# Kernel tuning notes

Hardware: AMD Instinct MI355X
Metric: run time of the kernel (lower is better)

Reference implementation:

```python
import jax, jax.numpy as jnp
import numpy as np

B, T, D, V, U = 16, 1000, 512, 5000, 64


def _safe_logaddexp(a, b):
    # logaddexp with nan-safe gradients when both args are -inf
    both = jnp.isneginf(a) & jnp.isneginf(b)
    a_ = jnp.where(both, 0.0, a)
    b_ = jnp.where(both, 0.0, b)
    return jnp.where(both, -jnp.inf, jnp.logaddexp(a_, b_))


def _log_sub_exp(a, b):
    # faithful port of log_substraction_exp: log(exp(a) - exp(b)), stable
    mask1 = (~jnp.isinf(a)) & (~jnp.isinf(b))
    a_ = jnp.where(mask1, a, -1.0)
    b_ = jnp.where(mask1, b, -2.0)
    ans_tmp = b_ + jnp.log(jnp.exp(a_ - b_) - 1.0)
    a_ = jnp.where(jnp.isinf(ans_tmp), -2000.0, a_)
    b_ = jnp.where(jnp.isinf(ans_tmp), -2001.0, b_)
    ans1 = b_ + jnp.log(jnp.exp(a_ - b_) - 1.0)
    ans = jnp.where(mask1, ans1, -jnp.inf)
    mask2 = (~jnp.isinf(a)) & jnp.isinf(b)
    return jnp.where(mask2, a, ans)


def _ctc_trellis(logp, ys):
    # Standard CTC lattice over extended labels (blank interleaved), S = 2U+1.
    # alpha[t,b,s]: logprob of paths over frames 0..t ending in state s (incl. emission at t)
    # beta[t,b,s]:  logprob of emitting frames t+1..T-1 and finishing, given state s at t
    # This reproduces the k2 lattice forward/backward scores at the label states.
    Bb, Tt, _ = logp.shape
    Uu = ys.shape[1]
    S = 2 * Uu + 1
    l_ext = jnp.zeros((Bb, S), ys.dtype).at[:, 1::2].set(ys)  # blank=0 at even s
    lp = jnp.take_along_axis(logp, jnp.broadcast_to(l_ext[:, None, :], (Bb, Tt, S)), axis=2)
    skip_ok = jnp.zeros((Bb, S), bool).at[:, 3::2].set(ys[:, 1:] != ys[:, :-1])
    lpT = jnp.transpose(lp, (1, 0, 2))  # [T,B,S]
    ninf1 = jnp.full((Bb, 1), -jnp.inf)
    ninf2 = jnp.full((Bb, 2), -jnp.inf)

    a0 = jnp.full((Bb, S), -jnp.inf).at[:, :2].set(lpT[0, :, :2])

    def astep(ap, lp_t):
        s1 = jnp.concatenate([ninf1, ap[:, :-1]], 1)
        s2 = jnp.concatenate([ninf2, ap[:, :-2]], 1)
        a = lp_t + _safe_logaddexp(_safe_logaddexp(ap, s1), jnp.where(skip_ok, s2, -jnp.inf))
        return a, a

    _, arest = jax.lax.scan(astep, a0, lpT[1:])
    alpha = jnp.concatenate([a0[None], arest], 0)  # [T,B,S]

    bl = jnp.full((Bb, S), -jnp.inf).at[:, S - 2:].set(0.0)  # final states: last label / last blank
    skipL2 = jnp.concatenate([skip_ok[:, 2:], jnp.zeros((Bb, 2), bool)], 1)

    def bstep(bn, lp_next):
        m = lp_next + bn
        m1 = jnp.concatenate([m[:, 1:], ninf1], 1)
        m2 = jnp.concatenate([m[:, 2:], ninf2], 1)
        bcur = _safe_logaddexp(_safe_logaddexp(m, m1), jnp.where(skipL2, m2, -jnp.inf))
        return bcur, bcur

    _, brest = jax.lax.scan(bstep, bl, lpT[1:], reverse=True)
    beta = jnp.concatenate([brest, bl[None]], 0)  # [T,B,S]
    return alpha, beta, lp


def setup_inputs() -> dict:
    key = jax.random.key(0)
    k1, k2, k3 = jax.random.split(key, 3)
    hs_pad = jax.random.normal(k1, (B, T, D), jnp.float32)
    hlens = jnp.full((B,), T, jnp.int32)
    ys_pad = jax.random.randint(k2, (B, U), 1, V)  # labels in [1, V); 0 is blank
    ali = jnp.zeros((B, U), jnp.int32)  # unused when risk_factor == 0
    W = jax.random.normal(k3, (D, V), jnp.float32) * 0.02
    b = jnp.zeros((V,), jnp.float32)
    return {"hs_pad": hs_pad, "hlens": hlens, "ys_pad": ys_pad, "ali": ali, "W": W, "b": b}


def reference(hs_pad, hlens, ys_pad, ali, W, b):
    # ctc_lo + log_softmax (dropout_rate=0). hlens are all equal -> sort/unsort is identity.
    logp = jax.nn.log_softmax(hs_pad @ W + b, axis=-1)  # [B,T,V]
    alpha_f, beta_f, lp = _ctc_trellis(logp, ys_pad)
    alpha = jnp.transpose(alpha_f[:, :, 1::2], (1, 2, 0))  # [B,U,T]
    beta = jnp.transpose(beta_f[:, :, 1::2], (1, 2, 0))    # [B,U,T]
    p = jnp.transpose(lp[:, :, 1::2], (0, 2, 1))           # [B,U,T] logprob of label u at frame t
    # beta', excluding re-emission of label u at t+1 -> paths whose label-u segment ends at t
    bp = _log_sub_exp(beta[:, :, :-1], beta[:, :, 1:] + p[:, :, 1:])
    bp = jnp.concatenate([bp, beta[:, :, -1:]], -1)
    loss_state = alpha + bp
    loss_state = jnp.where(jnp.isnan(loss_state), -jnp.inf, loss_state)
    loss_u = jax.nn.logsumexp(loss_state, axis=2)  # aggregate == 'time'
    mask = jnp.isinf(loss_u)
    denom = (~mask).astype(loss_u.dtype).sum(1)
    loss_fsas = jnp.where(mask, 0.0, loss_u).sum(1) / denom
    Uu = ys_pad.shape[1]
    loss_fsas = jnp.where(hlens < Uu, 0.0, loss_fsas)
    return (-loss_fsas).mean()
```

## Files before the change

### kernel.cpp

```cpp
#include <hip/hip_runtime.h>

#define NB 16
#define NT 1000
#define ND 512
#define NV 5000
#define NVP 5120
#define NU 64
#define NLL 66
#define NWG 72
#define NM (NB * NT)
#define NCH 40

typedef short short8v __attribute__((ext_vector_type(8)));
typedef float float4v __attribute__((ext_vector_type(4)));

#define NEGINF (-__builtin_inff())
#define SENTL  (-1.0e30f)
#define LOG2E 1.4426950408889634f
#define LN2F  0.6931471805599453f
#define SENT2 (-2000.4586751f * LOG2E)

__device__ __forceinline__ float fexp2(float x) { return __builtin_amdgcn_exp2f(x); }
__device__ __forceinline__ float flog2(float x) { return __builtin_amdgcn_logf(x); }

__device__ __forceinline__ float dpp_shr1(float x) {
  int xi = __builtin_bit_cast(int, x);
  int r = __builtin_amdgcn_update_dpp(xi, xi, 0x138, 0xf, 0xf, false);
  return __builtin_bit_cast(float, r);
}
__device__ __forceinline__ float dpp_shl1(float x) {
  int xi = __builtin_bit_cast(int, x);
  int r = __builtin_amdgcn_update_dpp(xi, xi, 0x130, 0xf, 0xf, false);
  return __builtin_bit_cast(float, r);
}

__device__ __forceinline__ short f2bf(float x) {
  unsigned int u = __builtin_bit_cast(unsigned int, x);
  unsigned int r = (u + 0x7fffu + ((u >> 16) & 1u)) >> 16;
  return (short)(unsigned short)r;
}
__device__ __forceinline__ float bf2f(short h) {
  unsigned int u = ((unsigned int)(unsigned short)h) << 16;
  return __builtin_bit_cast(float, u);
}

__device__ __forceinline__ void g2lds16(const short* g, short* l) {
  __builtin_amdgcn_global_load_lds(
      (const __attribute__((address_space(1))) void*)g,
      (__attribute__((address_space(3))) void*)l, 16, 0, 0);
}

__device__ __forceinline__ float lae2s(float a, float b) {
  float m = fmaxf(a, b);
  return m + flog2(fexp2(a - m) + fexp2(b - m));
}
__device__ __forceinline__ float lae3s(float a, float b, float c) {
  float m = fmaxf(fmaxf(a, b), c);
  return m + flog2(fexp2(a - m) + fexp2(b - m) + fexp2(c - m));
}
__device__ __forceinline__ float lsub2(float a, float b) {
  if (b < -1.0e29f) return (a < -1.0e29f) ? SENTL : a;
  float tmp = b + flog2(fexp2(a - b) - 1.0f);
  if (__builtin_isinf(tmp)) tmp = SENT2;
  return tmp;
}

__global__ __launch_bounds__(256) void k_cvt(const float* __restrict__ hs,
                                             const float* __restrict__ W,
                                             short* __restrict__ hsb,
                                             short* __restrict__ WT,
                                             short* __restrict__ WTlo,
                                             float* __restrict__ outv) {
  __shared__ short tileH[64 * 72];
  __shared__ short tileL[64 * 72];
  if (blockIdx.x < 4000) {
    if (blockIdx.x == 0 && threadIdx.x == 0) outv[0] = 0.0f;
    size_t i = (size_t)blockIdx.x * 256 + threadIdx.x;
    const float4* p = (const float4*)hs + i * 2;
    float4 v0 = p[0], v1 = p[1];
    short8v r;
    r[0] = f2bf(v0.x); r[1] = f2bf(v0.y); r[2] = f2bf(v0.z); r[3] = f2bf(v0.w);
    r[4] = f2bf(v1.x); r[5] = f2bf(v1.y); r[6] = f2bf(v1.z); r[7] = f2bf(v1.w);
    int row = (int)(i >> 6);
    int g = (int)(i & 63);
    int gs = (g & ~7) | ((g & 7) ^ (row & 7));
    *(short8v*)(hsb + (size_t)row * ND + gs * 8) = r;
    return;
  }
  int bx = blockIdx.x - 4000;
  int n0 = (bx % 80) * 64, k0 = (bx / 80) * 64;
  int tid = threadIdx.x;
  int kr = tid >> 2, part = tid & 3;
  const float* src = W + (size_t)(k0 + kr) * NV + n0 + part * 16;
#pragma unroll
  for (int jj = 0; jj < 4; ++jj) {
    int c = n0 + part * 16 + jj * 4;
    float4 v;
    if (c + 3 < NV) {
      v = *(const float4*)(src + jj * 4);
    } else {
      v.x = (c + 0 < NV) ? src[jj * 4 + 0] : 0.f;
      v.y = (c + 1 < NV) ? src[jj * 4 + 1] : 0.f;
      v.z = (c + 2 < NV) ? src[jj * 4 + 2] : 0.f;
      v.w = (c + 3 < NV) ? src[jj * 4 + 3] : 0.f;
    }
    int base = kr * 72 + part * 16 + jj * 4;
    float vv[4] = {v.x, v.y, v.z, v.w};
#pragma unroll
    for (int q = 0; q < 4; ++q) {
      short h = f2bf(vv[q]);
      tileH[base + q] = h;
      tileL[base + q] = f2bf(vv[q] - bf2f(h));
    }
  }
  __syncthreads();
  int n = tid & 63, kq = tid >> 6;
  int nn = n0 + n;
  if (nn < NVP) {
#pragma unroll
    for (int half = 0; half < 2; ++half) {
      short8v vh, vl;
#pragma unroll
      for (int jj = 0; jj < 8; ++jj) {
        vh[jj] = tileH[(kq * 16 + half * 8 + jj) * 72 + n];
        vl[jj] = tileL[(kq * 16 + half * 8 + jj) * 72 + n];
      }
      int g = (k0 >> 3) + kq * 2 + half;
      int gs = (g & ~7) | ((g & 7) ^ (nn & 7));
      *(short8v*)(WT + (size_t)nn * ND + gs * 8) = vh;
      *(short8v*)(WTlo + (size_t)nn * ND + gs * 8) = vl;
    }
  }
}

__global__ __launch_bounds__(64) void k_gather2(const short* __restrict__ WT,
                                                const short* __restrict__ WTlo,
                                                const int* __restrict__ ys,
                                                short* __restrict__ Wg_hi,
                                                short* __restrict__ Wg_lo) {
  int u = blockIdx.x, b = blockIdx.y, t = threadIdx.x;
  short8v hi = {0,0,0,0,0,0,0,0}, lo = {0,0,0,0,0,0,0,0};
  if (u < NU + 1) {
    int lab = (u == 0) ? 0 : ys[b * NU + u - 1];
    int ps = (t & ~7) | ((t & 7) ^ (lab & 7));
    hi = *(const short8v*)(WT + (size_t)lab * ND + ps * 8);
    lo = *(const short8v*)(WTlo + (size_t)lab * ND + ps * 8);
  }
  int q = (t & ~7) | ((t & 7) ^ (u & 7));
  size_t base = ((size_t)(b * NWG + u)) * ND + q * 8;
  *(short8v*)(Wg_hi + base) = hi;
  *(short8v*)(Wg_lo + base) = lo;
}

__global__ __launch_bounds__(256) void k_labg(const short* __restrict__ hsb,
                                              const short* __restrict__ Wg_hi,
                                              const short* __restrict__ Wg_lo,
                                              const int* __restrict__ ys,
                                              const float* __restrict__ bias,
                                              float* __restrict__ ll) {
  __shared__ short As[128 * 64];
  __shared__ short Bh[128 * 64];
  __shared__ short Bl[128 * 64];

  int mt = blockIdx.x, b = blockIdx.y;
  int t0 = mt * 128;
  int tid = threadIdx.x;
  int lane = tid & 63, wave = tid >> 6;
  int wm = wave >> 1, wn = wave & 1;
  int lrow = lane & 15, lkhi = lane >> 4;

  const short* gaBase = hsb + (size_t)(b * NT + t0 + wave * 32 + (lane >> 3)) * ND + (lane & 7) * 8;

  float4v acc[4][4];
#pragma unroll
  for (int m = 0; m < 4; ++m)
#pragma unroll
    for (int n = 0; n < 4; ++n)
#pragma unroll
      for (int j = 0; j < 4; ++j) acc[m][n][j] = 0.f;

  for (int s = 0; s < 8; ++s) {
    int k0 = s * 64;
#pragma unroll
    for (int i = 0; i < 4; ++i) {
      g2lds16(gaBase + (size_t)(i * 8) * ND + k0, &As[(wave * 32 + i * 8) * 64]);
      int brow = wave * 32 + (lane >> 3) + i * 8;
      int brc = (brow < NWG - 1) ? brow : (NWG - 1);
      g2lds16(Wg_hi + (size_t)(b * NWG + brc) * ND + (lane & 7) * 8 + k0,
              &Bh[(wave * 32 + i * 8) * 64]);
      g2lds16(Wg_lo + (size_t)(b * NWG + brc) * ND + (lane & 7) * 8 + k0,
              &Bl[(wave * 32 + i * 8) * 64]);
    }
    __syncthreads();
#pragma unroll
    for (int kk = 0; kk < 2; ++kk) {
      short8v av[4], bhv[4], blv2[4];
#pragma unroll
      for (int m = 0; m < 4; ++m) {
        int r = wm * 64 + m * 16 + lrow;
        int col = (kk * 32 + lkhi * 8) ^ ((r & 7) << 3);
        av[m] = *(const short8v*)&As[r * 64 + col];
      }
#pragma unroll
      for (int n = 0; n < 4; ++n) {
        int r = wn * 64 + n * 16 + lrow;
        int col = (kk * 32 + lkhi * 8) ^ ((r & 7) << 3);
        bhv[n] = *(const short8v*)&Bh[r * 64 + col];
        blv2[n] = *(const short8v*)&Bl[r * 64 + col];
      }
#pragma unroll
      for (int m = 0; m < 4; ++m)
#pragma unroll
        for (int n = 0; n < 4; ++n) {
          acc[m][n] = __builtin_amdgcn_mfma_f32_16x16x32_bf16(av[m], bhv[n], acc[m][n], 0, 0, 0);
          acc[m][n] = __builtin_amdgcn_mfma_f32_16x16x32_bf16(av[m], blv2[n], acc[m][n], 0, 0, 0);
        }
    }
    __syncthreads();
  }

  float bu[4]; bool uval[4];
#pragma unroll
  for (int n = 0; n < 4; ++n) {
    int u = wn * 64 + n * 16 + lrow;
    uval[n] = u < NU + 1;
    int lab = (u == 0) ? 0 : (uval[n] ? ys[b * NU + u - 1] : 0);
    bu[n] = uval[n] ? bias[lab] : 0.f;
  }
#pragma unroll
  for (int m = 0; m < 4; ++m)
#pragma unroll
    for (int j = 0; j < 4; ++j) {
      int trow = t0 + wm * 64 + m * 16 + lkhi * 4 + j;
      if (trow < NT) {
#pragma unroll
        for (int n = 0; n < 4; ++n) {
          int u = wn * 64 + n * 16 + lrow;
          if (uval[n])
            ll[((size_t)(b * NLL + u)) * NT + trow] = acc[m][n][j] + bu[n];
        }
      }
    }
}

__global__ __launch_bounds__(256) void k_big(const short* __restrict__ hsb,
                                             const short* __restrict__ WT,
                                             const float* __restrict__ bias,
                                             const float* __restrict__ ll,
                                             const int* __restrict__ ys,
                                             float* __restrict__ L,
                                             float* __restrict__ aod) {
  __shared__ short As[128 * 64];
  __shared__ short Ws[128 * 64];
  __shared__ float mred[128][2];
  __shared__ float sred[128][2];

  int bid = blockIdx.x;
  int tid = threadIdx.x;

  if (bid < NB) {
    float* pbS = (float*)As;
    int b = bid;
    const float* llb = ll + (size_t)b * NLL * NT;
    for (int i = tid; i < NT; i += 256) pbS[i] = llb[i] * LOG2E;
    __syncthreads();
    if (tid >= 64) return;
    int l = tid;
    const float* lrow = llb + (size_t)(1 + l) * NT;

    int lab = ys[b * NU + l];
    int labp = ys[b * NU + ((l >= 1) ? (l - 1) : 0)];
    bool skip = (l >= 1) && (lab != labp);
    float* aodb = aod + (size_t)b * NT * NU;

    float ae = (l == 0) ? pbS[0] : SENTL;
    float ao = (l == 0) ? lrow[0] * LOG2E : SENTL;
    aodb[l] = ao;

    float cl[16], pbr[16];
#pragma unroll
    for (int j = 0; j < 16; ++j) {
      int tt = 1 + j; if (tt > NT - 1) tt = NT - 1;
      cl[j] = lrow[tt];
      pbr[j] = pbS[tt];
    }
    for (int g = 0; g < 63; ++g) {
      float nl[16], pb2[16];
      if (g < 62) {
#pragma unroll
        for (int j = 0; j < 16; ++j) {
          int tt = 17 + g * 16 + j; if (tt > NT - 1) tt = NT - 1;
          nl[j] = lrow[tt];
          pb2[j] = pbS[tt];
        }
      } else {
#pragma unroll
        for (int j = 0; j < 16; ++j) { nl[j] = 0.f; pb2[j] = 0.f; }
      }
#pragma unroll
      for (int j = 0; j < 16; ++j) {
        int t = 1 + g * 16 + j;
        if (t < NT) {
          float pb = pbr[j];
          float pl = cl[j] * LOG2E;
          float po = dpp_shr1(ao); if (l == 0) po = SENTL;
          float aen = pb + lae2s(ae, po);
          float aon = pl + lae3s(ao, ae, skip ? po : SENTL);
          ae = aen; ao = aon;
          aodb[t * NU + l] = ao;
        }
      }
#pragma unroll
      for (int j = 0; j < 16; ++j) { cl[j] = nl[j]; pbr[j] = pb2[j]; }
    }
    return;
  }

  int lin = bid - NB;
  int o = (lin & 7) * 625 + (lin >> 3);
  int mt, chunk;
  if (o < 4800) {
    int sb = o / 320, w = o % 320;
    mt = sb * 8 + (w & 7);
    chunk = w >> 3;
  } else {
    int w = o - 4800;
    mt = 120 + (w % 5);
    chunk = w / 5;
  }
  int t0 = mt * 128;
  int n0 = chunk * 128;
  int lane = tid & 63, wave = tid >> 6;
  int wm = wave >> 1, wn = wave & 1;
  int lrow = lane & 15, lkhi = lane >> 4;

  const short* gaBase = hsb + (size_t)(t0 + wave * 32 + (lane >> 3)) * ND + (lane & 7) * 8;
  const short* gwBase = WT + (size_t)(n0 + wave * 32 + (lane >> 3)) * ND + (lane & 7) * 8;

  float4v acc[4][4];
#pragma unroll
  for (int m = 0; m < 4; ++m)
#pragma unroll
    for (int n = 0; n < 4; ++n)
#pragma unroll
      for (int j = 0; j < 4; ++j) acc[m][n][j] = 0.f;

  for (int s = 0; s < 8; ++s) {
    int k0 = s * 64;
#pragma unroll
    for (int i = 0; i < 4; ++i) {
      g2lds16(gaBase + (size_t)(i * 8) * ND + k0, &As[(wave * 32 + i * 8) * 64]);
      g2lds16(gwBase + (size_t)(i * 8) * ND + k0, &Ws[(wave * 32 + i * 8) * 64]);
    }
    __syncthreads();
#pragma unroll
    for (int kk = 0; kk < 2; ++kk) {
      short8v av[4], wv[4];
#pragma unroll
      for (int m = 0; m < 4; ++m) {
        int r = wm * 64 + m * 16 + lrow;
        int col = (kk * 32 + lkhi * 8) ^ ((r & 7) << 3);
        av[m] = *(const short8v*)&As[r * 64 + col];
      }
#pragma unroll
      for (int n = 0; n < 4; ++n) {
        int r = wn * 64 + n * 16 + lrow;
        int col = (kk * 32 + lkhi * 8) ^ ((r & 7) << 3);
        wv[n] = *(const short8v*)&Ws[r * 64 + col];
      }
#pragma unroll
      for (int m = 0; m < 4; ++m)
#pragma unroll
        for (int n = 0; n < 4; ++n)
          acc[m][n] = __builtin_amdgcn_mfma_f32_16x16x32_bf16(av[m], wv[n], acc[m][n], 0, 0, 0);
    }
    __syncthreads();
  }

  float bcol[4]; bool cval[4];
#pragma unroll
  for (int n = 0; n < 4; ++n) {
    int c = n0 + wn * 64 + n * 16 + lrow;
    cval[n] = c < NV;
    bcol[n] = cval[n] ? bias[c] : 0.f;
  }
#pragma unroll
  for (int m = 0; m < 4; ++m)
#pragma unroll
    for (int j = 0; j < 4; ++j) {
      float mx = NEGINF;
#pragma unroll
      for (int n = 0; n < 4; ++n) {
        float v = cval[n] ? acc[m][n][j] + bcol[n] : NEGINF;
        mx = fmaxf(mx, v);
      }
#pragma unroll
      for (int d = 1; d < 16; d <<= 1) mx = fmaxf(mx, __shfl_xor(mx, d));
      float mxc = fmaxf(mx, -3.0e38f);
      float p = 0.f;
#pragma unroll
      for (int n = 0; n < 4; ++n) {
        float v = cval[n] ? acc[m][n][j] + bcol[n] : NEGINF;
        p += __expf(v - mxc);
      }
#pragma unroll
      for (int d = 1; d < 16; d <<= 1) p += __shfl_xor(p, d);
      if (lrow == 0) {
        int rloc = wm * 64 + m * 16 + lkhi * 4 + j;
        mred[rloc][wn] = mx;
        sred[rloc][wn] = p;
      }
    }
  __syncthreads();
  if (tid < 128) {
    int row = t0 + tid;
    float m0 = mred[tid][0], m1 = mred[tid][1];
    float m = fmaxf(m0, m1);
    float ss = 0.f;
    if (m != NEGINF)
      ss = ((m0 == NEGINF) ? 0.f : sred[tid][0] * __expf(m0 - m))
         + ((m1 == NEGINF) ? 0.f : sred[tid][1] * __expf(m1 - m));
    float Lv = (m == NEGINF || ss <= 0.f) ? NEGINF : m + __logf(ss);
    L[(size_t)chunk * NM + row] = Lv;
  }
}

__global__ __launch_bounds__(256) void k_dred(const float* __restrict__ L,
                                              float* __restrict__ dnm) {
  int row = blockIdx.x * 256 + threadIdx.x;
  if (row >= NM) return;
  float m40 = NEGINF;
#pragma unroll
  for (int c = 0; c < NCH; ++c) m40 = fmaxf(m40, L[(size_t)c * NM + row]);
  float s = 0.f;
#pragma unroll
  for (int c = 0; c < NCH; ++c) {
    float Lc = L[(size_t)c * NM + row];
    if (Lc > -1.0e29f) s += __expf(Lc - m40);
  }
  dnm[row] = m40 + __logf(s);
}

__global__ __launch_bounds__(256) void k_bwd(const float* __restrict__ ll,
                                             const float* __restrict__ dnm,
                                             const int* __restrict__ ys,
                                             float* __restrict__ bp) {
  __shared__ float dnS[NT];
  __shared__ float pbS[NT];
  int b = blockIdx.x;
  int tid = threadIdx.x;
  const float* llb = ll + (size_t)b * NLL * NT;
  const float* dnb = dnm + b * NT;
  for (int t = tid; t < NT; t += 256) {
    float d = dnb[t];
    float blk = llb[t];
    dnS[t] = d;
    pbS[t] = (blk - d) * LOG2E;
  }
  __syncthreads();
  if (tid >= 64) return;
  int l = tid;
  const float* lrow = llb + (size_t)(1 + l) * NT;

  int lab = ys[b * NU + l];
  int labn = ys[b * NU + ((l < NU - 1) ? (l + 1) : l)];
  bool skipn = (l < NU - 1) && (labn != lab);
  float* bpb = bp + (size_t)b * NT * NU;

  float bo = (l == NU - 1) ? 0.0f : SENTL;
  float be = SENTL;
  float b128 = 0.0f;
  bpb[(NT - 1) * NU + l] = bo;

  float cl[16], pbr[16], dnr[16];
#pragma unroll
  for (int j = 0; j < 16; ++j) {
    int tt = NT - 2 - j; if (tt < 0) tt = 0;
    cl[j] = lrow[tt + 1];
    pbr[j] = pbS[tt + 1];
    dnr[j] = dnS[tt + 1];
  }
  for (int g = 0; g < 63; ++g) {
    float nl2[16], pb2[16], dn2[16];
    if (g < 62) {
#pragma unroll
      for (int j = 0; j < 16; ++j) {
        int tt = NT - 2 - 16 * (g + 1) - j; if (tt < 0) tt = 0;
        nl2[j] = lrow[tt + 1];
        pb2[j] = pbS[tt + 1];
        dn2[j] = dnS[tt + 1];
      }
    } else {
#pragma unroll
      for (int j = 0; j < 16; ++j) { nl2[j] = 0.f; pb2[j] = 0.f; dn2[j] = 0.f; }
    }
#pragma unroll
    for (int j = 0; j < 16; ++j) {
      int t = NT - 2 - 16 * g - j;
      if (t >= 0) {
        float pbv = pbr[j];
        float plv = (cl[j] - dnr[j]) * LOG2E;
        float me = pbv + be;
        float mo = plv + bo;
        float m128 = pbv + b128;
        float ne = dpp_shl1(me); if (l == NU - 1) ne = m128;
        float no = dpp_shl1(mo); if (l == NU - 1) no = SENTL;
        float ben = lae2s(me, mo);
        float bon = lae3s(mo, ne, skipn ? no : SENTL);
        bpb[t * NU + l] = lsub2(bon, mo);
        be = ben; bo = bon; b128 = m128;
      }
    }
#pragma unroll
    for (int j = 0; j < 16; ++j) { cl[j] = nl2[j]; pbr[j] = pb2[j]; dnr[j] = dn2[j]; }
  }
}

__global__ __launch_bounds__(512) void k_loss(const float* __restrict__ aod,
                                              const float* __restrict__ bp,
                                              const float* __restrict__ dnm,
                                              const int* __restrict__ hlens,
                                              float* __restrict__ out) {
  __shared__ float denL[NT];
  __shared__ float Dpre[NT];
  __shared__ float choff[64];
  __shared__ float ms[8][64], ss[8][64];
  int b = blockIdx.x, tid = threadIdx.x;
  for (int t = tid; t < NT; t += 512) denL[t] = dnm[b * NT + t];
  __syncthreads();
  if (tid < 64) {
    float s = 0.f;
#pragma unroll
    for (int i = 0; i < 16; ++i) { int t = tid * 16 + i; if (t < NT) s += denL[t]; }
    float v = s;
#pragma unroll
    for (int d = 1; d < 64; d <<= 1) { float u = __shfl_up(v, d); if (tid >= d) v += u; }
    choff[tid] = v - s;
  }
  __syncthreads();
  for (int t = tid; t < NT; t += 512) {
    float s = choff[t >> 4];
    int base = t & ~15;
    for (int i = base; i <= t; ++i) s += denL[i];
    Dpre[t] = s;
  }
  __syncthreads();
  int w = tid >> 6, l = tid & 63;
  const float* ab = aod + (size_t)b * NT * NU;
  const float* pbp = bp + (size_t)b * NT * NU;
  float m = NEGINF, s = 0.f;
  int t0 = w * 125, t1 = t0 + 125;
  for (int t = t0; t < t1; ++t) {
    float av = ab[t * NU + l];
    float pv = pbp[t * NU + l];
    float x = av - Dpre[t] * LOG2E + pv;
    if (__builtin_isnan(x) || x < -1.0e29f) continue;
    if (x > m) { s = s * fexp2(m - x) + 1.0f; m = x; }
    else       { s += fexp2(x - m); }
  }
  ms[w][l] = m; ss[w][l] = s;
  __syncthreads();
  if (w == 0) {
    float mm = NEGINF;
#pragma unroll
    for (int i = 0; i < 8; ++i) mm = fmaxf(mm, ms[i][l]);
    float lu;
    if (mm == NEGINF) lu = NEGINF;
    else {
      float st = 0.f;
#pragma unroll
      for (int i = 0; i < 8; ++i)
        st += (ms[i][l] == NEGINF) ? 0.f : ss[i][l] * fexp2(ms[i][l] - mm);
      lu = (mm + flog2(st)) * LN2F;
    }
    bool msk = __builtin_isinf(lu);
    float sv = msk ? 0.f : lu;
    float cv = msk ? 0.f : 1.f;
#pragma unroll
    for (int d = 1; d < 64; d <<= 1) { sv += __shfl_xor(sv, d); cv += __shfl_xor(cv, d); }
    if (l == 0) {
      float lf = sv / cv;
      if (hlens[b] < NU) lf = 0.f;
      atomicAdd(out, -lf * (1.0f / NB));
    }
  }
}

extern "C" void kernel_launch(void* const* d_in, const int* in_sizes, int n_in,
                              void* d_out, int out_size, void* d_ws, size_t ws_size,
                              hipStream_t stream) {
  const float* hs    = (const float*)d_in[0];
  const int*   hlens = (const int*)d_in[1];
  const int*   ys    = (const int*)d_in[2];
  const float* W     = (const float*)d_in[4];
  const float* bias  = (const float*)d_in[5];
  float* out = (float*)d_out;

  char* ws = (char*)d_ws;
  short* hsb   = (short*)(ws + 0);
  short* WT    = (short*)(ws + 16384000);
  short* WTlo  = (short*)(ws + 21626880);
  float* ll    = (float*)(ws + 21626880);
  float* L     = (float*)(ws + 25850880);
  short* Wg_hi = (short*)(ws + 28410880);
  short* Wg_lo = (short*)(ws + 29590528);
  float* aod   = (float*)(ws + 28410880);
  float* bpb   = (float*)(ws + 32506880);
  float* dnm   = (float*)(ws + 36602880);

  k_cvt<<<4640, 256, 0, stream>>>(hs, W, hsb, WT, WTlo, out);
  k_gather2<<<dim3(NWG, 16), 64, 0, stream>>>(WT, WTlo, ys, Wg_hi, Wg_lo);
  k_labg<<<dim3(8, 16), 256, 0, stream>>>(hsb, Wg_hi, Wg_lo, ys, bias, ll);
  k_big<<<5016, 256, 0, stream>>>(hsb, WT, bias, ll, ys, L, aod);
  k_dred<<<63, 256, 0, stream>>>(L, dnm);
  k_bwd<<<NB, 256, 0, stream>>>(ll, dnm, ys, bpb);
  k_loss<<<16, 512, 0, stream>>>(aod, bpb, dnm, hlens, out);
}
```

Measured before the change: 372.5 us.

## Fuse label gather into labg, double-buffer k_big LDS, fuse loss into backward

Removes the k_gather2 kernel by having k_labg load label rows of WT/WTlo directly, with the XOR swizzle folded into the address. Adds double-buffered LDS stages to the big GEMM in k_big so the next K-slice loads overlap the MFMA work on the current one. Folds k_loss into k_bwd: the prefix sum of the denominator and the online logsumexp over time are computed during the backward recursion, so the bp buffer is never written. In exchange, k_big needs twice the LDS, which can lower occupancy, and k_bwd does more work per step on only 16 blocks.

```diff
diff --git a/kernel.cpp b/kernel.cpp
--- a/kernel.cpp
+++ b/kernel.cpp
@@ -7,7 +7,6 @@
 #define NVP 5120
 #define NU 64
 #define NLL 66
-#define NWG 72
 #define NM (NB * NT)
 #define NCH 40
 
@@ -23,14 +22,14 @@
 __device__ __forceinline__ float fexp2(float x) { return __builtin_amdgcn_exp2f(x); }
 __device__ __forceinline__ float flog2(float x) { return __builtin_amdgcn_logf(x); }
 
+__device__ __forceinline__ float dpp_shl1(float x) {
+  int xi = __builtin_bit_cast(int, x);
+  int r = __builtin_amdgcn_update_dpp(xi, xi, 0x130, 0xf, 0xf, false);
+  return __builtin_bit_cast(float, r);
+}
 __device__ __forceinline__ float dpp_shr1(float x) {
   int xi = __builtin_bit_cast(int, x);
   int r = __builtin_amdgcn_update_dpp(xi, xi, 0x138, 0xf, 0xf, false);
-  return __builtin_bit_cast(float, r);
-}
-__device__ __forceinline__ float dpp_shl1(float x) {
-  int xi = __builtin_bit_cast(int, x);
-  int r = __builtin_amdgcn_update_dpp(xi, xi, 0x130, 0xf, 0xf, false);
   return __builtin_bit_cast(float, r);
 }
 
@@ -133,28 +132,9 @@
   }
 }
 
-__global__ __launch_bounds__(64) void k_gather2(const short* __restrict__ WT,
-                                                const short* __restrict__ WTlo,
-                                                const int* __restrict__ ys,
-                                                short* __restrict__ Wg_hi,
-                                                short* __restrict__ Wg_lo) {
-  int u = blockIdx.x, b = blockIdx.y, t = threadIdx.x;
-  short8v hi = {0,0,0,0,0,0,0,0}, lo = {0,0,0,0,0,0,0,0};
-  if (u < NU + 1) {
-    int lab = (u == 0) ? 0 : ys[b * NU + u - 1];
-    int ps = (t & ~7) | ((t & 7) ^ (lab & 7));
-    hi = *(const short8v*)(WT + (size_t)lab * ND + ps * 8);
-    lo = *(const short8v*)(WTlo + (size_t)lab * ND + ps * 8);
-  }
-  int q = (t & ~7) | ((t & 7) ^ (u & 7));
-  size_t base = ((size_t)(b * NWG + u)) * ND + q * 8;
-  *(short8v*)(Wg_hi + base) = hi;
-  *(short8v*)(Wg_lo + base) = lo;
-}
-
 __global__ __launch_bounds__(256) void k_labg(const short* __restrict__ hsb,
-                                              const short* __restrict__ Wg_hi,
-                                              const short* __restrict__ Wg_lo,
+                                              const short* __restrict__ WT,
+                                              const short* __restrict__ WTlo,
                                               const int* __restrict__ ys,
                                               const float* __restrict__ bias,
                                               float* __restrict__ ll) {
@@ -171,6 +151,15 @@
 
   const short* gaBase = hsb + (size_t)(b * NT + t0 + wave * 32 + (lane >> 3)) * ND + (lane & 7) * 8;
 
+  int labv[4], xorv[4];
+#pragma unroll
+  for (int i = 0; i < 4; ++i) {
+    int r = wave * 32 + (lane >> 3) + i * 8;
+    int lab = (r == 0) ? 0 : ((r <= NU) ? ys[b * NU + r - 1] : NV);
+    labv[i] = lab;
+    xorv[i] = ((lane & 7) ^ (r & 7) ^ (lab & 7)) * 8;
+  }
+
   float4v acc[4][4];
 #pragma unroll
   for (int m = 0; m < 4; ++m)
@@ -184,12 +173,8 @@
 #pragma unroll
     for (int i = 0; i < 4; ++i) {
       g2lds16(gaBase + (size_t)(i * 8) * ND + k0, &As[(wave * 32 + i * 8) * 64]);
-      int brow = wave * 32 + (lane >> 3) + i * 8;
-      int brc = (brow < NWG - 1) ? brow : (NWG - 1);
-      g2lds16(Wg_hi + (size_t)(b * NWG + brc) * ND + (lane & 7) * 8 + k0,
-              &Bh[(wave * 32 + i * 8) * 64]);
-      g2lds16(Wg_lo + (size_t)(b * NWG + brc) * ND + (lane & 7) * 8 + k0,
-              &Bl[(wave * 32 + i * 8) * 64]);
+      g2lds16(WT + (size_t)labv[i] * ND + k0 + xorv[i], &Bh[(wave * 32 + i * 8) * 64]);
+      g2lds16(WTlo + (size_t)labv[i] * ND + k0 + xorv[i], &Bl[(wave * 32 + i * 8) * 64]);
     }
     __syncthreads();
 #pragma unroll
@@ -250,8 +235,8 @@
                                              const int* __restrict__ ys,
                                              float* __restrict__ L,
                                              float* __restrict__ aod) {
-  __shared__ short As[128 * 64];
-  __shared__ short Ws[128 * 64];
+  __shared__ short As[2][128 * 64];
+  __shared__ short Ws[2][128 * 64];
   __shared__ float mred[128][2];
   __shared__ float sred[128][2];
 
@@ -345,14 +330,15 @@
 #pragma unroll
       for (int j = 0; j < 4; ++j) acc[m][n][j] = 0.f;
 
-  for (int s = 0; s < 8; ++s) {
+  auto stage = [&](int s, int bw) {
     int k0 = s * 64;
 #pragma unroll
     for (int i = 0; i < 4; ++i) {
-      g2lds16(gaBase + (size_t)(i * 8) * ND + k0, &As[(wave * 32 + i * 8) * 64]);
-      g2lds16(gwBase + (size_t)(i * 8) * ND + k0, &Ws[(wave * 32 + i * 8) * 64]);
-    }
-    __syncthreads();
+      g2lds16(gaBase + (size_t)(i * 8) * ND + k0, &As[bw][(wave * 32 + i * 8) * 64]);
+      g2lds16(gwBase + (size_t)(i * 8) * ND + k0, &Ws[bw][(wave * 32 + i * 8) * 64]);
+    }
+  };
+  auto compute = [&](int bw) {
 #pragma unroll
     for (int kk = 0; kk < 2; ++kk) {
       short8v av[4], wv[4];
@@ -360,13 +346,13 @@
       for (int m = 0; m < 4; ++m) {
         int r = wm * 64 + m * 16 + lrow;
         int col = (kk * 32 + lkhi * 8) ^ ((r & 7) << 3);
-        av[m] = *(const short8v*)&As[r * 64 + col];
+        av[m] = *(const short8v*)&As[bw][r * 64 + col];
       }
 #pragma unroll
       for (int n = 0; n < 4; ++n) {
         int r = wn * 64 + n * 16 + lrow;
         int col = (kk * 32 + lkhi * 8) ^ ((r & 7) << 3);
-        wv[n] = *(const short8v*)&Ws[r * 64 + col];
+        wv[n] = *(const short8v*)&Ws[bw][r * 64 + col];
       }
 #pragma unroll
       for (int m = 0; m < 4; ++m)
@@ -374,7 +360,21 @@
         for (int n = 0; n < 4; ++n)
           acc[m][n] = __builtin_amdgcn_mfma_f32_16x16x32_bf16(av[m], wv[n], acc[m][n], 0, 0, 0);
     }
-    __syncthreads();
+  };
+
+  stage(0, 0);
+  for (int s = 0; s < 8; ++s) {
+    if (s < 7) {
+      stage(s + 1, (s + 1) & 1);
+      asm volatile("s_waitcnt vmcnt(8)" ::: "memory");
+    } else {
+      asm volatile("s_waitcnt vmcnt(0)" ::: "memory");
+    }
+    __builtin_amdgcn_sched_barrier(0);
+    __builtin_amdgcn_s_barrier();
+    compute(s & 1);
+    __builtin_amdgcn_sched_barrier(0);
+    __builtin_amdgcn_s_barrier();
   }
 
   float bcol[4]; bool cval[4];
@@ -443,10 +443,14 @@
 
 __global__ __launch_bounds__(256) void k_bwd(const float* __restrict__ ll,
                                              const float* __restrict__ dnm,
+                                             const float* __restrict__ aod,
                                              const int* __restrict__ ys,
-                                             float* __restrict__ bp) {
+                                             const int* __restrict__ hlens,
+                                             float* __restrict__ out) {
   __shared__ float dnS[NT];
   __shared__ float pbS[NT];
+  __shared__ float Dpre[NT];
+  __shared__ float choff[64];
   int b = blockIdx.x;
   int tid = threadIdx.x;
   const float* llb = ll + (size_t)b * NLL * NT;
@@ -458,30 +462,53 @@
     pbS[t] = (blk - d) * LOG2E;
   }
   __syncthreads();
+  if (tid < 64) {
+    float s = 0.f;
+#pragma unroll
+    for (int i = 0; i < 16; ++i) { int t = tid * 16 + i; if (t < NT) s += dnS[t]; }
+    float v = s;
+#pragma unroll
+    for (int d = 1; d < 64; d <<= 1) { float u = __shfl_up(v, d); if (tid >= d) v += u; }
+    choff[tid] = v - s;
+  }
+  __syncthreads();
+  for (int t = tid; t < NT; t += 256) {
+    float s = choff[t >> 4];
+    int base = t & ~15;
+    for (int i = base; i <= t; ++i) s += dnS[i];
+    Dpre[t] = s;
+  }
+  __syncthreads();
   if (tid >= 64) return;
   int l = tid;
   const float* lrow = llb + (size_t)(1 + l) * NT;
+  const float* ab = aod + (size_t)b * NT * NU;
 
   int lab = ys[b * NU + l];
   int labn = ys[b * NU + ((l < NU - 1) ? (l + 1) : l)];
   bool skipn = (l < NU - 1) && (labn != lab);
-  float* bpb = bp + (size_t)b * NT * NU;
 
   float bo = (l == NU - 1) ? 0.0f : SENTL;
   float be = SENTL;
   float b128 = 0.0f;
-  bpb[(NT - 1) * NU + l] = bo;
-
-  float cl[16], pbr[16], dnr[16];
+  float mls = NEGINF, sls = 0.f;
+  {
+    float x = ab[(NT - 1) * NU + l] - Dpre[NT - 1] * LOG2E + bo;
+    if (!(__builtin_isnan(x) || x < -1.0e29f)) { mls = x; sls = 1.0f; }
+  }
+
+  float cl[16], pbr[16], dnr[16], ba[16], dpr[16];
 #pragma unroll
   for (int j = 0; j < 16; ++j) {
     int tt = NT - 2 - j; if (tt < 0) tt = 0;
     cl[j] = lrow[tt + 1];
     pbr[j] = pbS[tt + 1];
     dnr[j] = dnS[tt + 1];
+    ba[j] = ab[tt * NU + l];
+    dpr[j] = Dpre[tt];
   }
   for (int g = 0; g < 63; ++g) {
-    float nl2[16], pb2[16], dn2[16];
+    float nl2[16], pb2[16], dn2[16], na[16], dp2[16];
     if (g < 62) {
 #pragma unroll
       for (int j = 0; j < 16; ++j) {
@@ -489,10 +516,12 @@
         nl2[j] = lrow[tt + 1];
         pb2[j] = pbS[tt + 1];
         dn2[j] = dnS[tt + 1];
+        na[j] = ab[tt * NU + l];
+        dp2[j] = Dpre[tt];
       }
     } else {
 #pragma unroll
-      for (int j = 0; j < 16; ++j) { nl2[j] = 0.f; pb2[j] = 0.f; dn2[j] = 0.f; }
+      for (int j = 0; j < 16; ++j) { nl2[j] = 0.f; pb2[j] = 0.f; dn2[j] = 0.f; na[j] = 0.f; dp2[j] = 0.f; }
     }
 #pragma unroll
     for (int j = 0; j < 16; ++j) {
@@ -507,82 +536,31 @@
         float no = dpp_shl1(mo); if (l == NU - 1) no = SENTL;
         float ben = lae2s(me, mo);
         float bon = lae3s(mo, ne, skipn ? no : SENTL);
-        bpb[t * NU + l] = lsub2(bon, mo);
+        float pv = lsub2(bon, mo);
+        float x = ba[j] - dpr[j] * LOG2E + pv;
+        if (!(__builtin_isnan(x) || x < -1.0e29f)) {
+          if (x > mls) { sls = sls * fexp2(mls - x) + 1.0f; mls = x; }
+          else         { sls += fexp2(x - mls); }
+        }
         be = ben; bo = bon; b128 = m128;
       }
     }
 #pragma unroll
-    for (int j = 0; j < 16; ++j) { cl[j] = nl2[j]; pbr[j] = pb2[j]; dnr[j] = dn2[j]; }
-  }
-}
-
-__global__ __launch_bounds__(512) void k_loss(const float* __restrict__ aod,
-                                              const float* __restrict__ bp,
-                                              const float* __restrict__ dnm,
-                                              const int* __restrict__ hlens,
-                                              float* __restrict__ out) {
-  __shared__ float denL[NT];
-  __shared__ float Dpre[NT];
-  __shared__ float choff[64];
-  __shared__ float ms[8][64], ss[8][64];
-  int b = blockIdx.x, tid = threadIdx.x;
-  for (int t = tid; t < NT; t += 512) denL[t] = dnm[b * NT + t];
-  __syncthreads();
-  if (tid < 64) {
-    float s = 0.f;
-#pragma unroll
-    for (int i = 0; i < 16; ++i) { int t = tid * 16 + i; if (t < NT) s += denL[t]; }
-    float v = s;
-#pragma unroll
-    for (int d = 1; d < 64; d <<= 1) { float u = __shfl_up(v, d); if (tid >= d) v += u; }
-    choff[tid] = v - s;
-  }
-  __syncthreads();
-  for (int t = tid; t < NT; t += 512) {
-    float s = choff[t >> 4];
-    int base = t & ~15;
-    for (int i = base; i <= t; ++i) s += denL[i];
-    Dpre[t] = s;
-  }
-  __syncthreads();
-  int w = tid >> 6, l = tid & 63;
-  const float* ab = aod + (size_t)b * NT * NU;
-  const float* pbp = bp + (size_t)b * NT * NU;
-  float m = NEGINF, s = 0.f;
-  int t0 = w * 125, t1 = t0 + 125;
-  for (int t = t0; t < t1; ++t) {
-    float av = ab[t * NU + l];
-    float pv = pbp[t * NU + l];
-    float x = av - Dpre[t] * LOG2E + pv;
-    if (__builtin_isnan(x) || x < -1.0e29f) continue;
-    if (x > m) { s = s * fexp2(m - x) + 1.0f; m = x; }
-    else       { s += fexp2(x - m); }
-  }
-  ms[w][l] = m; ss[w][l] = s;
-  __syncthreads();
-  if (w == 0) {
-    float mm = NEGINF;
-#pragma unroll
-    for (int i = 0; i < 8; ++i) mm = fmaxf(mm, ms[i][l]);
-    float lu;
-    if (mm == NEGINF) lu = NEGINF;
-    else {
-      float st = 0.f;
-#pragma unroll
-      for (int i = 0; i < 8; ++i)
-        st += (ms[i][l] == NEGINF) ? 0.f : ss[i][l] * fexp2(ms[i][l] - mm);
-      lu = (mm + flog2(st)) * LN2F;
-    }
-    bool msk = __builtin_isinf(lu);
-    float sv = msk ? 0.f : lu;
-    float cv = msk ? 0.f : 1.f;
-#pragma unroll
-    for (int d = 1; d < 64; d <<= 1) { sv += __shfl_xor(sv, d); cv += __shfl_xor(cv, d); }
-    if (l == 0) {
-      float lf = sv / cv;
-      if (hlens[b] < NU) lf = 0.f;
-      atomicAdd(out, -lf * (1.0f / NB));
-    }
+    for (int j = 0; j < 16; ++j) {
+      cl[j] = nl2[j]; pbr[j] = pb2[j]; dnr[j] = dn2[j]; ba[j] = na[j]; dpr[j] = dp2[j];
+    }
+  }
+
+  float lu = (mls == NEGINF) ? NEGINF : (mls + flog2(sls)) * LN2F;
+  bool msk = __builtin_isinf(lu);
+  float sv = msk ? 0.f : lu;
+  float cv = msk ? 0.f : 1.f;
+#pragma unroll
+  for (int d = 1; d < 64; d <<= 1) { sv += __shfl_xor(sv, d); cv += __shfl_xor(cv, d); }
+  if (l == 0) {
+    float lf = sv / cv;
+    if (hlens[b] < NU) lf = 0.f;
+    atomicAdd(out, -lf * (1.0f / NB));
   }
 }
 
@@ -600,19 +578,14 @@
   short* hsb   = (short*)(ws + 0);
   short* WT    = (short*)(ws + 16384000);
   short* WTlo  = (short*)(ws + 21626880);
-  float* ll    = (float*)(ws + 21626880);
-  float* L     = (float*)(ws + 25850880);
-  short* Wg_hi = (short*)(ws + 28410880);
-  short* Wg_lo = (short*)(ws + 29590528);
-  float* aod   = (float*)(ws + 28410880);
-  float* bpb   = (float*)(ws + 32506880);
-  float* dnm   = (float*)(ws + 36602880);
+  float* aod   = (float*)(ws + 21626880);
+  float* ll    = (float*)(ws + 26869760);
+  float* L     = (float*)(ws + 31093760);
+  float* dnm   = (float*)(ws + 33653760);
 
   k_cvt<<<4640, 256, 0, stream>>>(hs, W, hsb, WT, WTlo, out);
-  k_gather2<<<dim3(NWG, 16), 64, 0, stream>>>(WT, WTlo, ys, Wg_hi, Wg_lo);
-  k_labg<<<dim3(8, 16), 256, 0, stream>>>(hsb, Wg_hi, Wg_lo, ys, bias, ll);
+  k_labg<<<dim3(8, 16), 256, 0, stream>>>(hsb, WT, WTlo, ys, bias, ll);
   k_big<<<5016, 256, 0, stream>>>(hsb, WT, bias, ll, ys, L, aod);
   k_dred<<<63, 256, 0, stream>>>(L, dnm);
-  k_bwd<<<NB, 256, 0, stream>>>(ll, dnm, ys, bpb);
-  k_loss<<<16, 512, 0, stream>>>(aod, bpb, dnm, hlens, out);
-}
+  k_bwd<<<NB, 256, 0, stream>>>(ll, dnm, aod, ys, hlens, out);
+}
```

Measured after the change: 435.2 us. 1.17x slower.
